# Kernel optimization log

Hardware: AMD Instinct MI355X
Metric: run time of the kernel (lower is better)

The kernel has to match this reference:

```python
import jax, jax.numpy as jnp
import numpy as np

B, K, N, F, H = 20000, 10, 100000, 256, 128


def setup_inputs() -> dict:
    key = jax.random.key(0)
    ks = jax.random.split(key, 8)
    neighbors = jax.random.randint(ks[0], (B, K), 0, N)
    embed_table = jax.random.normal(ks[1], (N, F), dtype=jnp.float32)
    w = lambda k, shp: jax.random.normal(k, shp, dtype=jnp.float32) * 0.05
    return {
        "neighbors": neighbors,
        "embed_table": embed_table,
        "W1a": w(ks[2], (F, H)), "W1b": w(ks[3], (H, H)),
        "W2a": w(ks[4], (F, H)), "W2b": w(ks[5], (H, H)),
        "W3a": w(ks[6], (F, H)), "W3b": w(ks[7], (H, H)),
    }


def reference(neighbors, embed_table, W1a, W1b, W2a, W2b, W3a, W3b):
    # Gather each batch node's K sampled neighbor embeddings: [B, K, F]
    x = embed_table[neighbors]
    # Three MLP projections: Linear(F,H,no bias) -> tanh -> Linear(H,H,no bias)
    q = jnp.tanh(x @ W1a) @ W1b              # [B, K, H]  (att1)
    k = jnp.tanh(x @ W2a) @ W2b              # [B, K, H]  (att2)
    v = jnp.tanh(x @ W3a) @ W3b              # [B, K, H]  (att3)
    # Per-node attention over the K neighbors, softmax along last dim
    att = jax.nn.softmax(jnp.einsum('bid,bjd->bij', q, k), axis=-1)  # [B, K, K]
    # torch: sum over rows of (att @ v) -> contract both i and j
    out = jnp.einsum('bij,bjd->bd', att, v)  # [B, H]
    return out
```

## Files before the change

kernel.cpp:

```cpp
#include <hip/hip_runtime.h>
#include <hip/hip_bf16.h>

constexpr int B_ = 20000;
constexpr int K_ = 10;
constexpr int N_ = 100000;
constexpr int F_ = 256;
constexpr int H_ = 128;

typedef __attribute__((ext_vector_type(8))) short bf16x8;
typedef __attribute__((ext_vector_type(4))) float f32x4;
typedef __attribute__((ext_vector_type(4))) unsigned short ushort4v;

__device__ __forceinline__ unsigned short f2bf(float x) {
  unsigned int u = __builtin_bit_cast(unsigned int, x);
  unsigned int r = u + 0x7fffu + ((u >> 16) & 1u);
  return (unsigned short)(r >> 16);
}

__device__ __forceinline__ float bf2f(unsigned int u16) {
  return __builtin_bit_cast(float, u16 << 16);
}

__device__ __forceinline__ float fast_tanh(float x) {
  float e = __expf(2.0f * x);
  return 1.0f - 2.0f * __builtin_amdgcn_rcpf(e + 1.0f);
}

__global__ __launch_bounds__(256) void prep_kernel(
    const float* __restrict__ W1a, const float* __restrict__ W1b,
    const float* __restrict__ W2a, const float* __restrict__ W2b,
    const float* __restrict__ W3a, const float* __restrict__ W3b,
    unsigned short* __restrict__ wat, unsigned short* __restrict__ wbt) {
  const float* Wa[3] = {W1a, W2a, W3a};
  const float* Wb[3] = {W1b, W2b, W3b};
  int g = blockIdx.x * 256 + threadIdx.x;
  if (g < 3 * F_ * H_) {
    int p = g >> 15;
    int r = g & (F_ * H_ - 1);
    int h = r >> 8;
    int k = r & 255;
    wat[g] = f2bf(Wa[p][k * H_ + h]);
  } else {
    int g2 = g - 3 * F_ * H_;
    int p = g2 >> 14;
    int r = g2 & (H_ * H_ - 1);
    int h = r >> 7;
    int k = r & 127;
    wbt[g2] = f2bf(Wb[p][k * H_ + h]);
  }
}

constexpr int MT = 32;
constexpr int XS = F_ + 8;
constexpr int TS = H_ + 8;

__global__ __launch_bounds__(256, 4) void proj_kernel(
    const float* __restrict__ E,
    const unsigned short* __restrict__ wat,
    const unsigned short* __restrict__ wbt,
    unsigned short* __restrict__ qo, unsigned short* __restrict__ ko,
    unsigned short* __restrict__ vo) {
  __shared__ unsigned short xs[MT * XS];
  __shared__ unsigned short ts[MT * TS];

  const int tid = threadIdx.x;
  const int lane = tid & 63;
  const int w = tid >> 6;
  const int l15 = lane & 15;
  const int kg = lane >> 4;
  const int row0 = blockIdx.x * MT;

  {
    const float4* Eg = (const float4*)E;
#pragma unroll
    for (int it = 0; it < 8; ++it) {
      int i = tid + 256 * it;
      int r = i >> 6;
      int c4 = i & 63;
      float4 v = Eg[(size_t)(row0 + r) * (F_ / 4) + c4];
      ushort4v o;
      o.x = f2bf(v.x); o.y = f2bf(v.y); o.z = f2bf(v.z); o.w = f2bf(v.w);
      *(ushort4v*)&xs[r * XS + c4 * 4] = o;
    }
  }
  __syncthreads();

  unsigned short* const outp[3] = {qo, ko, vo};

  for (int p = 0; p < 3; ++p) {
    const unsigned short* __restrict__ wap = wat + p * (F_ * H_);
    const unsigned short* __restrict__ wbp = wbt + p * (H_ * H_);

    bf16x8 b1r[8][2];
#pragma unroll
    for (int k = 0; k < 8; ++k) {
      const int koff = k * 32 + kg * 8;
      b1r[k][0] = *(const bf16x8*)&wap[(w * 32 + l15) * F_ + koff];
      b1r[k][1] = *(const bf16x8*)&wap[(w * 32 + 16 + l15) * F_ + koff];
    }

    f32x4 acc[2][2];
#pragma unroll
    for (int rt = 0; rt < 2; ++rt)
#pragma unroll
      for (int c = 0; c < 2; ++c) acc[rt][c] = (f32x4)0.0f;

#pragma unroll
    for (int k = 0; k < 8; ++k) {
      const int koff = k * 32 + kg * 8;
      bf16x8 a0 = *(const bf16x8*)&xs[l15 * XS + koff];
      bf16x8 a1 = *(const bf16x8*)&xs[(16 + l15) * XS + koff];
      acc[0][0] = __builtin_amdgcn_mfma_f32_16x16x32_bf16(a0, b1r[k][0], acc[0][0], 0, 0, 0);
      acc[0][1] = __builtin_amdgcn_mfma_f32_16x16x32_bf16(a0, b1r[k][1], acc[0][1], 0, 0, 0);
      acc[1][0] = __builtin_amdgcn_mfma_f32_16x16x32_bf16(a1, b1r[k][0], acc[1][0], 0, 0, 0);
      acc[1][1] = __builtin_amdgcn_mfma_f32_16x16x32_bf16(a1, b1r[k][1], acc[1][1], 0, 0, 0);
    }

    bf16x8 b2r[4][2];
#pragma unroll
    for (int k = 0; k < 4; ++k) {
      const int koff = k * 32 + kg * 8;
      b2r[k][0] = *(const bf16x8*)&wbp[(w * 32 + l15) * H_ + koff];
      b2r[k][1] = *(const bf16x8*)&wbp[(w * 32 + 16 + l15) * H_ + koff];
    }

    unsigned short tv[2][2][4];
#pragma unroll
    for (int rt = 0; rt < 2; ++rt)
#pragma unroll
      for (int c = 0; c < 2; ++c)
#pragma unroll
        for (int r = 0; r < 4; ++r)
          tv[rt][c][r] = f2bf(fast_tanh(acc[rt][c][r]));

    __syncthreads();
#pragma unroll
    for (int rt = 0; rt < 2; ++rt)
#pragma unroll
      for (int c = 0; c < 2; ++c)
#pragma unroll
        for (int r = 0; r < 4; ++r)
          ts[(rt * 16 + kg * 4 + r) * TS + w * 32 + c * 16 + l15] = tv[rt][c][r];
    __syncthreads();

    f32x4 ac2[2][2];
#pragma unroll
    for (int rt = 0; rt < 2; ++rt)
#pragma unroll
      for (int c = 0; c < 2; ++c) ac2[rt][c] = (f32x4)0.0f;

#pragma unroll
    for (int k = 0; k < 4; ++k) {
      const int koff = k * 32 + kg * 8;
      bf16x8 a0 = *(const bf16x8*)&ts[l15 * TS + koff];
      bf16x8 a1 = *(const bf16x8*)&ts[(16 + l15) * TS + koff];
      ac2[0][0] = __builtin_amdgcn_mfma_f32_16x16x32_bf16(a0, b2r[k][0], ac2[0][0], 0, 0, 0);
      ac2[0][1] = __builtin_amdgcn_mfma_f32_16x16x32_bf16(a0, b2r[k][1], ac2[0][1], 0, 0, 0);
      ac2[1][0] = __builtin_amdgcn_mfma_f32_16x16x32_bf16(a1, b2r[k][0], ac2[1][0], 0, 0, 0);
      ac2[1][1] = __builtin_amdgcn_mfma_f32_16x16x32_bf16(a1, b2r[k][1], ac2[1][1], 0, 0, 0);
    }

    unsigned short* __restrict__ o = outp[p];
#pragma unroll
    for (int rt = 0; rt < 2; ++rt)
#pragma unroll
      for (int c = 0; c < 2; ++c)
#pragma unroll
        for (int r = 0; r < 4; ++r) {
          int n = row0 + rt * 16 + kg * 4 + r;
          o[(size_t)n * H_ + w * 32 + c * 16 + l15] = f2bf(ac2[rt][c][r]);
        }
  }
}

__global__ __launch_bounds__(256) void agg_kernel(
    const int* __restrict__ nbr,
    const unsigned short* __restrict__ qa,
    const unsigned short* __restrict__ ka,
    const unsigned short* __restrict__ va,
    float* __restrict__ out) {
  const int lane = threadIdx.x & 63;
  const int wv = threadIdx.x >> 6;
  const int b = blockIdx.x * 4 + wv;
  const int l15 = lane & 15;
  const int kg = lane >> 4;

  const int ni = nbr[b * K_ + (l15 < K_ ? l15 : 0)];

  f32x4 sc = (f32x4)0.0f;
#pragma unroll
  for (int k = 0; k < 4; ++k) {
    const int off = k * 32 + kg * 8;
    bf16x8 qf = *(const bf16x8*)&qa[(size_t)ni * H_ + off];
    bf16x8 kf = *(const bf16x8*)&ka[(size_t)ni * H_ + off];
    sc = __builtin_amdgcn_mfma_f32_16x16x32_bf16(qf, kf, sc, 0, 0, 0);
  }

  if (l15 >= K_) {
#pragma unroll
    for (int r = 0; r < 4; ++r) sc[r] = -3.0e38f;
  }

  float mx[4], e[4], sm[4];
#pragma unroll
  for (int r = 0; r < 4; ++r) mx[r] = sc[r];
#pragma unroll
  for (int st = 1; st < 16; st <<= 1)
#pragma unroll
    for (int r = 0; r < 4; ++r) mx[r] = fmaxf(mx[r], __shfl_xor(mx[r], st, 16));
#pragma unroll
  for (int r = 0; r < 4; ++r) { e[r] = __expf(sc[r] - mx[r]); sm[r] = e[r]; }
#pragma unroll
  for (int st = 1; st < 16; st <<= 1)
#pragma unroll
    for (int r = 0; r < 4; ++r) sm[r] += __shfl_xor(sm[r], st, 16);

  float cs = 0.0f;
#pragma unroll
  for (int r = 0; r < 4; ++r) {
    float a = e[r] * __builtin_amdgcn_rcpf(sm[r]);
    if (kg * 4 + r >= K_) a = 0.0f;
    cs += a;
  }
  cs += __shfl_xor(cs, 16, 64);
  cs += __shfl_xor(cs, 32, 64);

  float o0 = 0.0f, o1 = 0.0f;
#pragma unroll
  for (int j = 0; j < K_; ++j) {
    const float cj = __shfl(cs, j, 64);
    const int nj = __shfl(ni, j, 64);
    const unsigned int v2 = *(const unsigned int*)&va[(size_t)nj * H_ + 2 * lane];
    o0 = fmaf(cj, bf2f(v2 & 0xffffu), o0);
    o1 = fmaf(cj, bf2f(v2 >> 16), o1);
  }
  *(float2*)&out[(size_t)b * H_ + 2 * lane] = make_float2(o0, o1);
}

extern "C" void kernel_launch(void* const* d_in, const int* in_sizes, int n_in,
                              void* d_out, int out_size, void* d_ws, size_t ws_size,
                              hipStream_t stream) {
  const int* nbr = (const int*)d_in[0];
  const float* E = (const float*)d_in[1];
  const float* W1a = (const float*)d_in[2];
  const float* W1b = (const float*)d_in[3];
  const float* W2a = (const float*)d_in[4];
  const float* W2b = (const float*)d_in[5];
  const float* W3a = (const float*)d_in[6];
  const float* W3b = (const float*)d_in[7];
  float* out = (float*)d_out;

  unsigned short* qa = (unsigned short*)d_ws;
  unsigned short* ka = qa + (size_t)N_ * H_;
  unsigned short* va = ka + (size_t)N_ * H_;
  unsigned short* wat = va + (size_t)N_ * H_;
  unsigned short* wbt = wat + (size_t)3 * F_ * H_;

  prep_kernel<<<(3 * F_ * H_ + 3 * H_ * H_) / 256, 256, 0, stream>>>(
      W1a, W1b, W2a, W2b, W3a, W3b, wat, wbt);
  proj_kernel<<<N_ / MT, 256, 0, stream>>>(E, wat, wbt, qa, ka, va);
  agg_kernel<<<B_ / 4, 256, 0, stream>>>(nbr, qa, ka, va, out);
}
```

Measured before the change: 285.1 us.

## Split projection into two kernels with 32x32 MFMA and interleaved QKV buffer

```diff
diff --git a/kernel.cpp b/kernel.cpp
--- a/kernel.cpp
+++ b/kernel.cpp
@@ -6,9 +6,11 @@
 constexpr int N_ = 100000;
 constexpr int F_ = 256;
 constexpr int H_ = 128;
+constexpr int RW = 3 * H_;
 
 typedef __attribute__((ext_vector_type(8))) short bf16x8;
 typedef __attribute__((ext_vector_type(4))) float f32x4;
+typedef __attribute__((ext_vector_type(16))) float f32x16;
 typedef __attribute__((ext_vector_type(4))) unsigned short ushort4v;
 
 __device__ __forceinline__ unsigned short f2bf(float x) {
@@ -50,34 +52,31 @@
   }
 }
 
-constexpr int MT = 32;
+constexpr int MT = 64;
 constexpr int XS = F_ + 8;
-constexpr int TS = H_ + 8;
-
-__global__ __launch_bounds__(256, 4) void proj_kernel(
+
+__global__ __launch_bounds__(256) void proj1_kernel(
     const float* __restrict__ E,
     const unsigned short* __restrict__ wat,
-    const unsigned short* __restrict__ wbt,
-    unsigned short* __restrict__ qo, unsigned short* __restrict__ ko,
-    unsigned short* __restrict__ vo) {
+    unsigned short* __restrict__ qkvI) {
   __shared__ unsigned short xs[MT * XS];
-  __shared__ unsigned short ts[MT * TS];
 
   const int tid = threadIdx.x;
   const int lane = tid & 63;
   const int w = tid >> 6;
-  const int l15 = lane & 15;
-  const int kg = lane >> 4;
+  const int m = lane & 31;
+  const int hf = lane >> 5;
   const int row0 = blockIdx.x * MT;
 
   {
     const float4* Eg = (const float4*)E;
 #pragma unroll
-    for (int it = 0; it < 8; ++it) {
+    for (int it = 0; it < 16; ++it) {
       int i = tid + 256 * it;
       int r = i >> 6;
       int c4 = i & 63;
-      float4 v = Eg[(size_t)(row0 + r) * (F_ / 4) + c4];
+      float4 v = make_float4(0.f, 0.f, 0.f, 0.f);
+      if (row0 + r < N_) v = Eg[(size_t)(row0 + r) * (F_ / 4) + c4];
       ushort4v o;
       o.x = f2bf(v.x); o.y = f2bf(v.y); o.z = f2bf(v.z); o.w = f2bf(v.w);
       *(ushort4v*)&xs[r * XS + c4 * 4] = o;
@@ -85,99 +84,77 @@
   }
   __syncthreads();
 
-  unsigned short* const outp[3] = {qo, ko, vo};
-
   for (int p = 0; p < 3; ++p) {
     const unsigned short* __restrict__ wap = wat + p * (F_ * H_);
+
+    f32x16 acc0 = (f32x16)0.0f;
+    f32x16 acc1 = (f32x16)0.0f;
+
+#pragma unroll
+    for (int k = 0; k < 16; ++k) {
+      const int koff = k * 16 + hf * 8;
+      bf16x8 b = *(const bf16x8*)&wap[(w * 32 + m) * F_ + koff];
+      bf16x8 a0 = *(const bf16x8*)&xs[m * XS + koff];
+      bf16x8 a1 = *(const bf16x8*)&xs[(32 + m) * XS + koff];
+      acc0 = __builtin_amdgcn_mfma_f32_32x32x16_bf16(a0, b, acc0, 0, 0, 0);
+      acc1 = __builtin_amdgcn_mfma_f32_32x32x16_bf16(a1, b, acc1, 0, 0, 0);
+    }
+
+    const int col = p * H_ + w * 32 + m;
+#pragma unroll
+    for (int reg = 0; reg < 16; ++reg) {
+      int rr = (reg & 3) + 8 * (reg >> 2) + 4 * hf;
+      int n0 = row0 + rr;
+      int n1 = row0 + 32 + rr;
+      if (n0 < N_) qkvI[(size_t)n0 * RW + col] = f2bf(fast_tanh(acc0[reg]));
+      if (n1 < N_) qkvI[(size_t)n1 * RW + col] = f2bf(fast_tanh(acc1[reg]));
+    }
+  }
+}
+
+__global__ __launch_bounds__(256) void proj2_kernel(
+    const unsigned short* __restrict__ wbt,
+    unsigned short* __restrict__ qkvI) {
+  const int tid = threadIdx.x;
+  const int lane = tid & 63;
+  const int gw = (blockIdx.x * 256 + tid) >> 6;
+  const int row0 = gw * 16;
+  if (row0 >= N_) return;
+  const int l15 = lane & 15;
+  const int q4 = lane >> 4;
+
+  for (int p = 0; p < 3; ++p) {
     const unsigned short* __restrict__ wbp = wbt + p * (H_ * H_);
 
-    bf16x8 b1r[8][2];
-#pragma unroll
-    for (int k = 0; k < 8; ++k) {
-      const int koff = k * 32 + kg * 8;
-      b1r[k][0] = *(const bf16x8*)&wap[(w * 32 + l15) * F_ + koff];
-      b1r[k][1] = *(const bf16x8*)&wap[(w * 32 + 16 + l15) * F_ + koff];
-    }
-
-    f32x4 acc[2][2];
-#pragma unroll
-    for (int rt = 0; rt < 2; ++rt)
-#pragma unroll
-      for (int c = 0; c < 2; ++c) acc[rt][c] = (f32x4)0.0f;
-
-#pragma unroll
-    for (int k = 0; k < 8; ++k) {
-      const int koff = k * 32 + kg * 8;
-      bf16x8 a0 = *(const bf16x8*)&xs[l15 * XS + koff];
-      bf16x8 a1 = *(const bf16x8*)&xs[(16 + l15) * XS + koff];
-      acc[0][0] = __builtin_amdgcn_mfma_f32_16x16x32_bf16(a0, b1r[k][0], acc[0][0], 0, 0, 0);
-      acc[0][1] = __builtin_amdgcn_mfma_f32_16x16x32_bf16(a0, b1r[k][1], acc[0][1], 0, 0, 0);
-      acc[1][0] = __builtin_amdgcn_mfma_f32_16x16x32_bf16(a1, b1r[k][0], acc[1][0], 0, 0, 0);
-      acc[1][1] = __builtin_amdgcn_mfma_f32_16x16x32_bf16(a1, b1r[k][1], acc[1][1], 0, 0, 0);
-    }
-
-    bf16x8 b2r[4][2];
+    f32x4 acc[8];
+#pragma unroll
+    for (int c = 0; c < 8; ++c) acc[c] = (f32x4)0.0f;
+
+    const size_t abase = (size_t)(row0 + l15) * RW + p * H_;
 #pragma unroll
     for (int k = 0; k < 4; ++k) {
-      const int koff = k * 32 + kg * 8;
-      b2r[k][0] = *(const bf16x8*)&wbp[(w * 32 + l15) * H_ + koff];
-      b2r[k][1] = *(const bf16x8*)&wbp[(w * 32 + 16 + l15) * H_ + koff];
-    }
-
-    unsigned short tv[2][2][4];
-#pragma unroll
-    for (int rt = 0; rt < 2; ++rt)
-#pragma unroll
-      for (int c = 0; c < 2; ++c)
-#pragma unroll
-        for (int r = 0; r < 4; ++r)
-          tv[rt][c][r] = f2bf(fast_tanh(acc[rt][c][r]));
-
-    __syncthreads();
-#pragma unroll
-    for (int rt = 0; rt < 2; ++rt)
-#pragma unroll
-      for (int c = 0; c < 2; ++c)
-#pragma unroll
-        for (int r = 0; r < 4; ++r)
-          ts[(rt * 16 + kg * 4 + r) * TS + w * 32 + c * 16 + l15] = tv[rt][c][r];
-    __syncthreads();
-
-    f32x4 ac2[2][2];
-#pragma unroll
-    for (int rt = 0; rt < 2; ++rt)
-#pragma unroll
-      for (int c = 0; c < 2; ++c) ac2[rt][c] = (f32x4)0.0f;
-
-#pragma unroll
-    for (int k = 0; k < 4; ++k) {
-      const int koff = k * 32 + kg * 8;
-      bf16x8 a0 = *(const bf16x8*)&ts[l15 * TS + koff];
-      bf16x8 a1 = *(const bf16x8*)&ts[(16 + l15) * TS + koff];
-      ac2[0][0] = __builtin_amdgcn_mfma_f32_16x16x32_bf16(a0, b2r[k][0], ac2[0][0], 0, 0, 0);
-      ac2[0][1] = __builtin_amdgcn_mfma_f32_16x16x32_bf16(a0, b2r[k][1], ac2[0][1], 0, 0, 0);
-      ac2[1][0] = __builtin_amdgcn_mfma_f32_16x16x32_bf16(a1, b2r[k][0], ac2[1][0], 0, 0, 0);
-      ac2[1][1] = __builtin_amdgcn_mfma_f32_16x16x32_bf16(a1, b2r[k][1], ac2[1][1], 0, 0, 0);
-    }
-
-    unsigned short* __restrict__ o = outp[p];
-#pragma unroll
-    for (int rt = 0; rt < 2; ++rt)
-#pragma unroll
-      for (int c = 0; c < 2; ++c)
-#pragma unroll
-        for (int r = 0; r < 4; ++r) {
-          int n = row0 + rt * 16 + kg * 4 + r;
-          o[(size_t)n * H_ + w * 32 + c * 16 + l15] = f2bf(ac2[rt][c][r]);
-        }
+      const int koff = k * 32 + q4 * 8;
+      bf16x8 a = *(const bf16x8*)&qkvI[abase + koff];
+#pragma unroll
+      for (int c = 0; c < 8; ++c) {
+        bf16x8 b = *(const bf16x8*)&wbp[(c * 16 + l15) * H_ + koff];
+        acc[c] = __builtin_amdgcn_mfma_f32_16x16x32_bf16(a, b, acc[c], 0, 0, 0);
+      }
+    }
+
+#pragma unroll
+    for (int c = 0; c < 8; ++c)
+#pragma unroll
+      for (int r = 0; r < 4; ++r) {
+        int n = row0 + q4 * 4 + r;
+        qkvI[(size_t)n * RW + p * H_ + c * 16 + l15] = f2bf(acc[c][r]);
+      }
   }
 }
 
 __global__ __launch_bounds__(256) void agg_kernel(
     const int* __restrict__ nbr,
-    const unsigned short* __restrict__ qa,
-    const unsigned short* __restrict__ ka,
-    const unsigned short* __restrict__ va,
+    const unsigned short* __restrict__ qkvI,
     float* __restrict__ out) {
   const int lane = threadIdx.x & 63;
   const int wv = threadIdx.x >> 6;
@@ -186,13 +163,14 @@
   const int kg = lane >> 4;
 
   const int ni = nbr[b * K_ + (l15 < K_ ? l15 : 0)];
+  const size_t nbase = (size_t)ni * RW;
 
   f32x4 sc = (f32x4)0.0f;
 #pragma unroll
   for (int k = 0; k < 4; ++k) {
     const int off = k * 32 + kg * 8;
-    bf16x8 qf = *(const bf16x8*)&qa[(size_t)ni * H_ + off];
-    bf16x8 kf = *(const bf16x8*)&ka[(size_t)ni * H_ + off];
+    bf16x8 qf = *(const bf16x8*)&qkvI[nbase + off];
+    bf16x8 kf = *(const bf16x8*)&qkvI[nbase + H_ + off];
     sc = __builtin_amdgcn_mfma_f32_16x16x32_bf16(qf, kf, sc, 0, 0, 0);
   }
 
@@ -230,7 +208,8 @@
   for (int j = 0; j < K_; ++j) {
     const float cj = __shfl(cs, j, 64);
     const int nj = __shfl(ni, j, 64);
-    const unsigned int v2 = *(const unsigned int*)&va[(size_t)nj * H_ + 2 * lane];
+    const unsigned int v2 =
+        *(const unsigned int*)&qkvI[(size_t)nj * RW + 2 * H_ + 2 * lane];
     o0 = fmaf(cj, bf2f(v2 & 0xffffu), o0);
     o1 = fmaf(cj, bf2f(v2 >> 16), o1);
   }
@@ -250,14 +229,13 @@
   const float* W3b = (const float*)d_in[7];
   float* out = (float*)d_out;
 
-  unsigned short* qa = (unsigned short*)d_ws;
-  unsigned short* ka = qa + (size_t)N_ * H_;
-  unsigned short* va = ka + (size_t)N_ * H_;
-  unsigned short* wat = va + (size_t)N_ * H_;
+  unsigned short* qkvI = (unsigned short*)d_ws;
+  unsigned short* wat = qkvI + (size_t)N_ * RW;
   unsigned short* wbt = wat + (size_t)3 * F_ * H_;
 
   prep_kernel<<<(3 * F_ * H_ + 3 * H_ * H_) / 256, 256, 0, stream>>>(
       W1a, W1b, W2a, W2b, W3a, W3b, wat, wbt);
-  proj_kernel<<<N_ / MT, 256, 0, stream>>>(E, wat, wbt, qa, ka, va);
-  agg_kernel<<<B_ / 4, 256, 0, stream>>>(nbr, qa, ka, va, out);
-}
+  proj1_kernel<<<(N_ + MT - 1) / MT, 256, 0, stream>>>(E, wat, qkvI);
+  proj2_kernel<<<(N_ / 16 + 3) / 4, 256, 0, stream>>>(wbt, qkvI);
+  agg_kernel<<<B_ / 4, 256, 0, stream>>>(nbr, qkvI, out);
+}
```

After: 353.4 us. +24.0%, slower.
